# Performance work log

Hardware: AMD Instinct MI355X
Metric: run time of the kernel (lower is better)

Reference implementation:

```python
import jax, jax.numpy as jnp
import numpy as np


def setup_inputs() -> dict:
    key = jax.random.key(0)
    k1, k2 = jax.random.split(key)
    B, N, M = 16, 4096, 4096
    array1 = jax.random.normal(k1, (B, N, 3), dtype=jnp.float32)
    array2 = jax.random.normal(k2, (B, M, 3), dtype=jnp.float32)
    return {"array1": array1, "array2": array2}


def reference(array1, array2):
    # Squared pairwise distances via ||x||^2 + ||y||^2 - 2<x,y>  -> [B, N, M]
    x2 = jnp.sum(array1 * array1, axis=-1)  # [B, N]
    y2 = jnp.sum(array2 * array2, axis=-1)  # [B, M]
    xy = jnp.einsum("bnc,bmc->bnm", array1, array2)  # [B, N, M]
    d = x2[:, :, None] + y2[None if False else slice(None), None, :] - 2.0 * xy
    d = jnp.maximum(d, 0.0)  # clamp fp round-off negatives (dists are squared)
    dist1 = jnp.min(d, axis=2)  # [B, N] squared NN dist array1 -> array2
    dist2 = jnp.min(d, axis=1)  # [B, M] squared NN dist array2 -> array1
    dist = jnp.mean(jnp.sqrt(dist1)) + jnp.mean(jnp.sqrt(dist2))
    return dist / 2.0 * 1000.0
```

## Files before the change

### kernel.cpp

```cpp
#include <hip/hip_runtime.h>
#include <math.h>

#define NB    16
#define NP    4096
#define BXR   128
#define NBLK  (NB * (NP / BXR) * 2)

typedef _Float16 f16;
typedef _Float16 f16x4  __attribute__((ext_vector_type(4)));
typedef _Float16 f16x8  __attribute__((ext_vector_type(8)));
typedef float    f32x16 __attribute__((ext_vector_type(16)));

__global__ __launch_bounds__(256, 4) void chamfer_mfma_kernel(
    const float* __restrict__ A1, const float* __restrict__ A2,
    float* __restrict__ part)
{
    __shared__ f16x4 sy[NP];
    __shared__ float sacc[4];
    const int b   = blockIdx.x;
    const int xc  = blockIdx.y;
    const int dir = blockIdx.z;
    const float* X = dir ? A2 : A1;
    const float* Y = dir ? A1 : A2;

    const int tid  = threadIdx.x;
    const int lane = tid & 63;
    const int w    = tid >> 6;
    const int col  = lane & 31;

    const float* Yb = Y + (size_t)b * NP * 3;
    for (int i = tid; i < NP; i += 256) {
        const float fx = Yb[3 * i], fy = Yb[3 * i + 1], fz = Yb[3 * i + 2];
        const f16 hx = (f16)fx, hy = (f16)fy, hz = (f16)fz;
        const float xx = (float)hx, yy = (float)hy, zz = (float)hz;
        sy[i] = (f16x4){hx, hy, hz, (f16)(-0.5f * (xx * xx + yy * yy + zz * zz))};
    }

    const int xbase = xc * BXR + w * 32;
    const float* p = X + ((size_t)b * NP + xbase + col) * 3;
    const f16 ahx = (f16)p[0], ahy = (f16)p[1], ahz = (f16)p[2];
    const float axx = (float)ahx, ayy = (float)ahy, azz = (float)ahz;
    const float nax = -0.5f * (axx * axx + ayy * ayy + azz * azz);
    f16x8 bfr = (f16x8)(f16)0.f;
    if (lane < 32)
        bfr = (f16x8){ahx, ahy, ahz, (f16)1.0f,
                      (f16)0.f, (f16)0.f, (f16)0.f, (f16)0.f};
    __syncthreads();

    f32x16 mx;
    #pragma unroll
    for (int r = 0; r < 16; ++r) mx[r] = -3.3e38f;
    const f32x16 Z = {};

    f16x4 q0 = sy[col];
    f16x4 q1 = sy[32 + col];
    #pragma unroll 2
    for (int j = 0; j < NP / 64; ++j) {
        const int jn = (j + 1) & (NP / 64 - 1);
        const f16x4 p0 = sy[jn * 64 + col];
        const f16x4 p1 = sy[jn * 64 + 32 + col];
        const f16x8 a0 = __builtin_shufflevector(q0, q0, 0, 1, 2, 3, -1, -1, -1, -1);
        const f16x8 a1 = __builtin_shufflevector(q1, q1, 0, 1, 2, 3, -1, -1, -1, -1);
        const f32x16 d0 =
            __builtin_amdgcn_mfma_f32_32x32x16_f16(a0, bfr, Z, 0, 0, 0);
        const f32x16 d1 =
            __builtin_amdgcn_mfma_f32_32x32x16_f16(a1, bfr, Z, 0, 0, 0);
        #pragma unroll
        for (int r = 0; r < 16; ++r)
            mx[r] = fmaxf(fmaxf(mx[r], d0[r]), d1[r]);
        q0 = p0; q1 = p1;
    }

    #define F3(a, bb, c) fmaxf(fmaxf((a), (bb)), (c))
    const float t0 = F3(mx[0],  mx[1],  mx[2]);
    const float t1 = F3(mx[3],  mx[4],  mx[5]);
    const float t2 = F3(mx[6],  mx[7],  mx[8]);
    const float t3 = F3(mx[9],  mx[10], mx[11]);
    const float t4 = F3(mx[12], mx[13], mx[14]);
    float v = fmaxf(F3(t0, t1, t2), F3(t3, t4, mx[15]));
    #undef F3
    v = fmaxf(v, __shfl_xor(v, 32, 64));

    const float e = fmaxf(-(nax + v), 0.0f);
    float s = (lane < 32) ? sqrtf(2.0f * e) : 0.0f;
    #pragma unroll
    for (int off = 32; off > 0; off >>= 1)
        s += __shfl_down(s, off, 64);

    if (lane == 0) sacc[w] = s;
    __syncthreads();
    if (tid == 0) {
        const int bid = blockIdx.x + NB * (blockIdx.y + (NP / BXR) * blockIdx.z);
        part[bid] = (sacc[0] + sacc[1]) + (sacc[2] + sacc[3]);
    }
}

__global__ __launch_bounds__(1024) void final_reduce_kernel(
    const float* __restrict__ part, float* __restrict__ out)
{
    float s = part[threadIdx.x];
    #pragma unroll
    for (int off = 32; off > 0; off >>= 1)
        s += __shfl_down(s, off, 64);

    __shared__ float ws[16];
    const int lane = threadIdx.x & 63;
    const int wid  = threadIdx.x >> 6;
    if (lane == 0) ws[wid] = s;
    __syncthreads();
    if (threadIdx.x == 0) {
        float t = 0.0f;
        #pragma unroll
        for (int v = 0; v < 16; ++v) t += ws[v];
        out[0] = t * 0.00762939453125f;
    }
}

extern "C" void kernel_launch(void* const* d_in, const int* in_sizes, int n_in,
                              void* d_out, int out_size, void* d_ws, size_t ws_size,
                              hipStream_t stream)
{
    const float* a1 = (const float*)d_in[0];
    const float* a2 = (const float*)d_in[1];
    float* out = (float*)d_out;
    float* part = (float*)d_ws;

    dim3 grid(NB, NP / BXR, 2);
    chamfer_mfma_kernel<<<grid, 256, 0, stream>>>(a1, a2, part);

    final_reduce_kernel<<<1, 1024, 0, stream>>>(part, out);
}
```

Measured before the change: 74.29 us.

## Register-block two X tiles per wave to reuse Y fragments across MFMAs

Each wave now processes 64 query points instead of 32, using two B fragments and two running-max accumulators. Each LDS-loaded Y fragment therefore feeds four MFMAs instead of two. Doubling the block tile to 256 points halves the grid, so the per-block staging of all Y points into shared memory is paid half as often. The final reduce is resized to the smaller partial count. The cost is more registers and fewer blocks, with occupancy lowered to 2 per SIMD, which may hide latency less well.

```diff
diff --git a/kernel.cpp b/kernel.cpp
--- a/kernel.cpp
+++ b/kernel.cpp
@@ -3,7 +3,7 @@
 
 #define NB    16
 #define NP    4096
-#define BXR   128
+#define BXR   256
 #define NBLK  (NB * (NP / BXR) * 2)
 
 typedef _Float16 f16;
@@ -11,7 +11,7 @@
 typedef _Float16 f16x8  __attribute__((ext_vector_type(8)));
 typedef float    f32x16 __attribute__((ext_vector_type(16)));
 
-__global__ __launch_bounds__(256, 4) void chamfer_mfma_kernel(
+__global__ __launch_bounds__(256, 2) void chamfer_mfma_kernel(
     const float* __restrict__ A1, const float* __restrict__ A2,
     float* __restrict__ part)
 {
@@ -36,20 +36,27 @@
         sy[i] = (f16x4){hx, hy, hz, (f16)(-0.5f * (xx * xx + yy * yy + zz * zz))};
     }
 
-    const int xbase = xc * BXR + w * 32;
-    const float* p = X + ((size_t)b * NP + xbase + col) * 3;
-    const f16 ahx = (f16)p[0], ahy = (f16)p[1], ahz = (f16)p[2];
-    const float axx = (float)ahx, ayy = (float)ahy, azz = (float)ahz;
-    const float nax = -0.5f * (axx * axx + ayy * ayy + azz * azz);
-    f16x8 bfr = (f16x8)(f16)0.f;
-    if (lane < 32)
-        bfr = (f16x8){ahx, ahy, ahz, (f16)1.0f,
-                      (f16)0.f, (f16)0.f, (f16)0.f, (f16)0.f};
+    const int xbase = xc * BXR + w * 64;
+    const float* p0 = X + ((size_t)b * NP + xbase + col) * 3;
+    const float* p1 = X + ((size_t)b * NP + xbase + 32 + col) * 3;
+    const f16 h0x = (f16)p0[0], h0y = (f16)p0[1], h0z = (f16)p0[2];
+    const f16 h1x = (f16)p1[0], h1y = (f16)p1[1], h1z = (f16)p1[2];
+    const float a0x = (float)h0x, a0y = (float)h0y, a0z = (float)h0z;
+    const float a1x = (float)h1x, a1y = (float)h1y, a1z = (float)h1z;
+    const float nax0 = -0.5f * (a0x * a0x + a0y * a0y + a0z * a0z);
+    const float nax1 = -0.5f * (a1x * a1x + a1y * a1y + a1z * a1z);
+    f16x8 bfr0 = (f16x8)(f16)0.f, bfr1 = (f16x8)(f16)0.f;
+    if (lane < 32) {
+        bfr0 = (f16x8){h0x, h0y, h0z, (f16)1.0f,
+                       (f16)0.f, (f16)0.f, (f16)0.f, (f16)0.f};
+        bfr1 = (f16x8){h1x, h1y, h1z, (f16)1.0f,
+                       (f16)0.f, (f16)0.f, (f16)0.f, (f16)0.f};
+    }
     __syncthreads();
 
-    f32x16 mx;
+    f32x16 mx0, mx1;
     #pragma unroll
-    for (int r = 0; r < 16; ++r) mx[r] = -3.3e38f;
+    for (int r = 0; r < 16; ++r) { mx0[r] = -3.3e38f; mx1[r] = -3.3e38f; }
     const f32x16 Z = {};
 
     f16x4 q0 = sy[col];
@@ -57,32 +64,49 @@
     #pragma unroll 2
     for (int j = 0; j < NP / 64; ++j) {
         const int jn = (j + 1) & (NP / 64 - 1);
-        const f16x4 p0 = sy[jn * 64 + col];
-        const f16x4 p1 = sy[jn * 64 + 32 + col];
-        const f16x8 a0 = __builtin_shufflevector(q0, q0, 0, 1, 2, 3, -1, -1, -1, -1);
-        const f16x8 a1 = __builtin_shufflevector(q1, q1, 0, 1, 2, 3, -1, -1, -1, -1);
-        const f32x16 d0 =
-            __builtin_amdgcn_mfma_f32_32x32x16_f16(a0, bfr, Z, 0, 0, 0);
-        const f32x16 d1 =
-            __builtin_amdgcn_mfma_f32_32x32x16_f16(a1, bfr, Z, 0, 0, 0);
+        const f16x4 n0 = sy[jn * 64 + col];
+        const f16x4 n1 = sy[jn * 64 + 32 + col];
+        const f16x8 a0 = __builtin_shufflevector(q0, q1, 0, 1, 2, 3, 4, 5, 6, 7);
+        const f16x8 a1 = __builtin_shufflevector(q1, q0, 0, 1, 2, 3, 4, 5, 6, 7);
+        const f32x16 d00 =
+            __builtin_amdgcn_mfma_f32_32x32x16_f16(a0, bfr0, Z, 0, 0, 0);
+        const f32x16 d10 =
+            __builtin_amdgcn_mfma_f32_32x32x16_f16(a1, bfr0, Z, 0, 0, 0);
+        const f32x16 d01 =
+            __builtin_amdgcn_mfma_f32_32x32x16_f16(a0, bfr1, Z, 0, 0, 0);
+        const f32x16 d11 =
+            __builtin_amdgcn_mfma_f32_32x32x16_f16(a1, bfr1, Z, 0, 0, 0);
         #pragma unroll
-        for (int r = 0; r < 16; ++r)
-            mx[r] = fmaxf(fmaxf(mx[r], d0[r]), d1[r]);
-        q0 = p0; q1 = p1;
+        for (int r = 0; r < 16; ++r) {
+            mx0[r] = fmaxf(fmaxf(mx0[r], d00[r]), d10[r]);
+            mx1[r] = fmaxf(fmaxf(mx1[r], d01[r]), d11[r]);
+        }
+        q0 = n0; q1 = n1;
     }
 
     #define F3(a, bb, c) fmaxf(fmaxf((a), (bb)), (c))
-    const float t0 = F3(mx[0],  mx[1],  mx[2]);
-    const float t1 = F3(mx[3],  mx[4],  mx[5]);
-    const float t2 = F3(mx[6],  mx[7],  mx[8]);
-    const float t3 = F3(mx[9],  mx[10], mx[11]);
-    const float t4 = F3(mx[12], mx[13], mx[14]);
-    float v = fmaxf(F3(t0, t1, t2), F3(t3, t4, mx[15]));
+    float v0, v1;
+    {
+        const float t0 = F3(mx0[0],  mx0[1],  mx0[2]);
+        const float t1 = F3(mx0[3],  mx0[4],  mx0[5]);
+        const float t2 = F3(mx0[6],  mx0[7],  mx0[8]);
+        const float t3 = F3(mx0[9],  mx0[10], mx0[11]);
+        const float t4 = F3(mx0[12], mx0[13], mx0[14]);
+        v0 = fmaxf(F3(t0, t1, t2), F3(t3, t4, mx0[15]));
+        const float u0 = F3(mx1[0],  mx1[1],  mx1[2]);
+        const float u1 = F3(mx1[3],  mx1[4],  mx1[5]);
+        const float u2 = F3(mx1[6],  mx1[7],  mx1[8]);
+        const float u3 = F3(mx1[9],  mx1[10], mx1[11]);
+        const float u4 = F3(mx1[12], mx1[13], mx1[14]);
+        v1 = fmaxf(F3(u0, u1, u2), F3(u3, u4, mx1[15]));
+    }
     #undef F3
-    v = fmaxf(v, __shfl_xor(v, 32, 64));
+    v0 = fmaxf(v0, __shfl_xor(v0, 32, 64));
+    v1 = fmaxf(v1, __shfl_xor(v1, 32, 64));
 
-    const float e = fmaxf(-(nax + v), 0.0f);
-    float s = (lane < 32) ? sqrtf(2.0f * e) : 0.0f;
+    const float e0 = fmaxf(-(nax0 + v0), 0.0f);
+    const float e1 = fmaxf(-(nax1 + v1), 0.0f);
+    float s = (lane < 32) ? (sqrtf(2.0f * e0) + sqrtf(2.0f * e1)) : 0.0f;
     #pragma unroll
     for (int off = 32; off > 0; off >>= 1)
         s += __shfl_down(s, off, 64);
@@ -95,7 +119,7 @@
     }
 }
 
-__global__ __launch_bounds__(1024) void final_reduce_kernel(
+__global__ __launch_bounds__(512) void final_reduce_kernel(
     const float* __restrict__ part, float* __restrict__ out)
 {
     float s = part[threadIdx.x];
@@ -103,7 +127,7 @@
     for (int off = 32; off > 0; off >>= 1)
         s += __shfl_down(s, off, 64);
 
-    __shared__ float ws[16];
+    __shared__ float ws[8];
     const int lane = threadIdx.x & 63;
     const int wid  = threadIdx.x >> 6;
     if (lane == 0) ws[wid] = s;
@@ -111,7 +135,7 @@
     if (threadIdx.x == 0) {
         float t = 0.0f;
         #pragma unroll
-        for (int v = 0; v < 16; ++v) t += ws[v];
+        for (int v = 0; v < 8; ++v) t += ws[v];
         out[0] = t * 0.00762939453125f;
     }
 }
@@ -128,5 +152,5 @@
     dim3 grid(NB, NP / BXR, 2);
     chamfer_mfma_kernel<<<grid, 256, 0, stream>>>(a1, a2, part);
 
-    final_reduce_kernel<<<1, 1024, 0, stream>>>(part, out);
+    final_reduce_kernel<<<1, 512, 0, stream>>>(part, out);
 }
```

After: 74.93 us. No clear change (+0.9%).
